# Kernel optimization log

Measured on AMD Instinct MI355X. Metric: run time of the kernel, lower is better.

The kernel has to match this reference:

```python
import jax, jax.numpy as jnp
import numpy as np

N_NONZERO = 32      # n_nonzero_coefs
TAU = 0.01
LAMBDA_INIT = -5.0  # reg_coeff = softplus(lambda)


def setup_inputs() -> dict:
    key = jax.random.key(0)
    k1, k2 = jax.random.split(key)
    X = jax.random.normal(k1, (64, 1024, 1024), dtype=jnp.float32)
    y = jax.random.normal(k2, (64, 1024, 1), dtype=jnp.float32)
    return {"X": X, "y": y}


def _omp_fit_forward(X, y):
    # Faithful translation of fit() (omp with hard straight-through top-1)
    # followed by forward() reconstruction D @ coef.
    reg = jax.nn.softplus(jnp.asarray(LAMBDA_INIT, jnp.float32)).astype(X.dtype)
    B, L, A = X.shape
    ones = jnp.ones((B, L, 1), X.dtype)
    Dfull = jnp.concatenate([X, ones], axis=-1)   # [B, L, A+1] (bias column)
    D = Dfull[0]                                   # shared dictionary [L, A+1]
    n_atoms = A + 1
    y2 = y[:, :, 0]                                # [B, L]
    y_det = jax.lax.stop_gradient(y2)
    residuals = y_det
    # Cache selected_D columns incrementally: each column j is dict @ ret_j,
    # identical math to the original's full recompute every iteration.
    selD = jnp.zeros((B, L, N_NONZERO), X.dtype)
    idx_all = []
    nzW = None
    for i in range(N_NONZERO):
        proj = residuals @ D                                      # [B, A+1]
        soft = jax.nn.softmax(jnp.abs(proj) / TAU, axis=-1)
        idx = jnp.argmax(jnp.abs(proj), axis=-1)                  # detached indices
        onehot = jax.nn.one_hot(jnp.argmax(soft, axis=-1), n_atoms, dtype=X.dtype)
        ret = onehot - jax.lax.stop_gradient(soft) + soft         # straight-through
        new_col = ret @ D.T                                       # [B, L]
        selD = selD.at[:, :, i].set(new_col)
        Di = selD[:, :, :i + 1]                                   # [B, L, i+1]
        DTy = jnp.einsum('blk,bl->bk', Di, y2)[..., None]         # [B, i+1, 1]
        DTD = jnp.einsum('blk,blj->bkj', Di, Di) + reg * jnp.eye(i + 1, dtype=X.dtype)
        nzW = jnp.linalg.solve(DTD, DTy)                          # [B, i+1, 1]
        residuals = y_det - jnp.einsum('blk,bk->bl', Di, nzW[..., 0])
        idx_all.append(idx)
    indices = jnp.stack(idx_all, axis=1)                          # [B, K] int
    W = jnp.zeros((B, n_atoms), X.dtype).at[jnp.arange(B)[:, None], indices].set(nzW[..., 0])
    # forward(): bmm(dict_with_bias, coef)
    recon = jnp.einsum('bla,ba->bl', Dfull, W)[..., None]         # [B, L, 1]
    return recon


def reference(X, y):
    return _omp_fit_forward(X, y)
```

## Files before the change

### kernel.cpp

```cpp
#include <hip/hip_runtime.h>
#include <math.h>

#define NATOMS   1025
#define GSTRIDE  1040
#define GELEMS   (1025*GSTRIDE)
#define CSTRIDE  33
#define NNZ      32
#define NBATCH   64
#define REGL     0.0067153485f

#define DPPF(x, ctrl) __int_as_float(__builtin_amdgcn_update_dpp(0, __float_as_int(x), (ctrl), 0xF, 0xF, false))

__device__ __forceinline__ float wave_sum64(float x) {
    x += DPPF(x, 0x111);
    x += DPPF(x, 0x112);
    x += DPPF(x, 0x114);
    x += DPPF(x, 0x118);
    x += DPPF(x, 0x142);
    x += DPPF(x, 0x143);
    return __int_as_float(__builtin_amdgcn_readlane(__float_as_int(x), 63));
}
__device__ __forceinline__ float readlane_f(float x, int l) {
    return __int_as_float(__builtin_amdgcn_readlane(__float_as_int(x), l));
}

__global__ __launch_bounds__(256)
void gramprojy_kernel(const float* __restrict__ X0, const float* __restrict__ y,
                      float* __restrict__ Gout, float* __restrict__ PY,
                      int kLen, int nsplit) {
    __shared__ float lds[8192];
    const int tid = threadIdx.x;

    if ((int)blockIdx.z < nsplit) {
        const int bx = blockIdx.x, by = blockIdx.y, bz = blockIdx.z;
        if (by < bx) return;
        float* As = lds;
        float* Bs = lds + 4096;
        const int a0 = bx * 128, b0 = by * 128;
        float* __restrict__ Gp = Gout + (size_t)bz * GELEMS;
        const int tx = tid & 15;
        const int ty = tid >> 4;
        const int lr = tid >> 5;
        const int lc = (tid & 31) * 4;
        const bool aIn = (a0 + 128) <= 1024;
        const bool bIn = (b0 + 128) <= 1024;

        float acc[8][8];
#pragma unroll
        for (int m = 0; m < 8; ++m)
#pragma unroll
            for (int n = 0; n < 8; ++n) acc[m][n] = 0.0f;

        const int kBase = bz * kLen;
        for (int kc = 0; kc < kLen; kc += 32) {
#pragma unroll
            for (int rr = 0; rr < 4; ++rr) {
                const int r = lr + rr * 8;
                const int l = kBase + kc + r;
                if (aIn) {
                    *(float4*)&As[r * 128 + lc] = *(const float4*)&X0[(size_t)l * 1024 + a0 + lc];
                } else {
#pragma unroll
                    for (int k = 0; k < 4; ++k) {
                        const int col = a0 + lc + k;
                        As[r * 128 + lc + k] = (col < 1024) ? X0[(size_t)l * 1024 + col]
                                                            : (col == 1024 ? 1.0f : 0.0f);
                    }
                }
                if (bIn) {
                    *(float4*)&Bs[r * 128 + lc] = *(const float4*)&X0[(size_t)l * 1024 + b0 + lc];
                } else {
#pragma unroll
                    for (int k = 0; k < 4; ++k) {
                        const int col = b0 + lc + k;
                        Bs[r * 128 + lc + k] = (col < 1024) ? X0[(size_t)l * 1024 + col]
                                                            : (col == 1024 ? 1.0f : 0.0f);
                    }
                }
            }
            __syncthreads();
#pragma unroll 8
            for (int l = 0; l < 32; ++l) {
                float4 a01 = *(const float4*)&As[l * 128 + ty * 8];
                float4 a23 = *(const float4*)&As[l * 128 + ty * 8 + 4];
                float4 bA  = *(const float4*)&Bs[l * 128 + tx * 4];
                float4 bB  = *(const float4*)&Bs[l * 128 + 64 + tx * 4];
                float am[8] = {a01.x, a01.y, a01.z, a01.w, a23.x, a23.y, a23.z, a23.w};
                float bn[8] = {bA.x, bA.y, bA.z, bA.w, bB.x, bB.y, bB.z, bB.w};
#pragma unroll
                for (int m = 0; m < 8; ++m)
#pragma unroll
                    for (int n = 0; n < 8; ++n)
                        acc[m][n] += am[m] * bn[n];
            }
            __syncthreads();
        }

#pragma unroll
        for (int m = 0; m < 8; ++m) {
            const int a = a0 + ty * 8 + m;
            if (a >= NATOMS) continue;
            const int bAc = b0 + tx * 4;
            const int bBc = b0 + 64 + tx * 4;
            if (bAc < GSTRIDE) {
                *(float4*)&Gp[(size_t)a * GSTRIDE + bAc] =
                    make_float4(acc[m][0], acc[m][1], acc[m][2], acc[m][3]);
            }
            if (bBc < GSTRIDE) {
                *(float4*)&Gp[(size_t)a * GSTRIDE + bBc] =
                    make_float4(acc[m][4], acc[m][5], acc[m][6], acc[m][7]);
            }
        }
        if (bx != by) {
#pragma unroll
            for (int n = 0; n < 8; ++n) {
                const int colg = b0 + ((n < 4) ? (tx * 4 + n) : (64 + tx * 4 + (n - 4)));
                if (colg >= NATOMS) continue;
                const int a = a0 + ty * 8;
                *(float4*)&Gp[(size_t)colg * GSTRIDE + a] =
                    make_float4(acc[0][n], acc[1][n], acc[2][n], acc[3][n]);
                *(float4*)&Gp[(size_t)colg * GSTRIDE + a + 4] =
                    make_float4(acc[4][n], acc[5][n], acc[6][n], acc[7][n]);
            }
        }
    } else {
        const int pw = blockIdx.y * 9 + blockIdx.x;
        if (pw >= 68) return;
        const int a0 = (pw % 17) * 64;
        const int b0 = (pw / 17) * 16;
        float* Ds = lds;
        float* Ys = lds + 2048;
        const int tx = tid & 15;
        const int ty = tid >> 4;
        const bool aIn = (a0 + 64) <= 1024;

        float acc[4] = {0.0f, 0.0f, 0.0f, 0.0f};

        for (int kc = 0; kc < 1024; kc += 32) {
            {
                const int r  = tid >> 4;
                const int c4 = (tid & 15) * 4;
#pragma unroll
                for (int rr = 0; rr < 2; ++rr) {
                    const int row = r + rr * 16;
                    const int l = kc + row;
                    if (aIn) {
                        *(float4*)&Ds[row * 64 + c4] = *(const float4*)&X0[(size_t)l * 1024 + a0 + c4];
                    } else {
#pragma unroll
                        for (int k = 0; k < 4; ++k) {
                            const int col = a0 + c4 + k;
                            Ds[row * 64 + c4 + k] = (col < 1024) ? X0[(size_t)l * 1024 + col]
                                                                 : (col == 1024 ? 1.0f : 0.0f);
                        }
                    }
                }
            }
            for (int e = tid; e < 512; e += 256) {
                const int l = e & 31, bb = e >> 5;
                Ys[l * 17 + bb] = y[(size_t)(b0 + bb) * 1024 + kc + l];
            }
            __syncthreads();
#pragma unroll 8
            for (int l = 0; l < 32; ++l) {
                const float yv = Ys[l * 17 + ty];
                float4 dv = *(const float4*)&Ds[l * 64 + tx * 4];
                acc[0] += yv * dv.x; acc[1] += yv * dv.y;
                acc[2] += yv * dv.z; acc[3] += yv * dv.w;
            }
            __syncthreads();
        }
        const int a = a0 + tx * 4;
        if (a < GSTRIDE) {
            *(float4*)&PY[(size_t)(b0 + ty) * GSTRIDE + a] =
                make_float4(acc[0], acc[1], acc[2], acc[3]);
        }
    }
}

template <int NS>
__global__ __launch_bounds__(512)
void omp_kernel(const float* __restrict__ Gp, const float* __restrict__ PY,
                int* __restrict__ idxOut, float* __restrict__ wOut) {
    __shared__ float colT[NATOMS * CSTRIDE];
    __shared__ float pyLds[1040];
    __shared__ float diagLds[1040];
    __shared__ float redV[2][8];
    __shared__ int   redI[2][8];

    const int b = blockIdx.x, tid = threadIdx.x;
    const int lane = tid & 63, wid = tid >> 6;

    float rr0[NNZ], rr1[NNZ];
    float ainv[32];
#pragma unroll
    for (int m = 0; m < 32; ++m) { ainv[m] = 0.f; rr0[m] = 0.f; rr1[m] = 0.f; }
    float wvr = 0.f, rhsr = 0.f;
    int   myIdx = 0;

    {
        for (int u = tid; u < NATOMS * CSTRIDE; u += 512) colT[u] = 0.f;
        const float* pyg = PY + (size_t)b * GSTRIDE;
        pyLds[tid] = pyg[tid];
        pyLds[tid + 512] = pyg[tid + 512];
        if (tid < 16) pyLds[1024 + tid] = pyg[1024 + tid];
        float d0 = 0.f, d1 = 0.f, d2 = 0.f;
#pragma unroll
        for (int z = 0; z < NS; ++z) {
            const float* gz = Gp + (size_t)z * GELEMS;
            d0 += gz[(size_t)tid * (GSTRIDE + 1)];
            d1 += gz[(size_t)(tid + 512) * (GSTRIDE + 1)];
            if (tid == 511) d2 += gz[(size_t)1024 * (GSTRIDE + 1)];
        }
        diagLds[tid] = d0;
        diagLds[tid + 512] = d1;
        if (tid == 511) diagLds[1024] = d2;
    }
    __syncthreads();

    float p0 = pyLds[tid], p1 = pyLds[tid + 512];
    float p2 = (tid == 511) ? pyLds[1024] : 0.f;

#define AM_STEP(ctrl) {                                                        \
        float ov = DPPF(wv_, ctrl);                                            \
        int   oi = __builtin_amdgcn_update_dpp(0, wi_, (ctrl), 0xF, 0xF, false);\
        if (ov > wv_ || (ov == wv_ && oi < wi_)) { wv_ = ov; wi_ = oi; } }
    {
        float best = fabsf(p0); int bidx = tid;
        { float v = fabsf(p1); if (v > best) { best = v; bidx = tid + 512; } }
        if (tid == 511) { float v = fabsf(p2); if (v > best) { best = v; bidx = 1024; } }
        float wv_ = best; int wi_ = bidx;
        AM_STEP(0x111) AM_STEP(0x112) AM_STEP(0x114) AM_STEP(0x118)
        AM_STEP(0x142) AM_STEP(0x143)
        wv_ = readlane_f(wv_, 63);
        wi_ = __builtin_amdgcn_readlane(wi_, 63);
        if (lane == 0) { redV[0][wid] = wv_; redI[0][wid] = wi_; }
    }
    __syncthreads();

#define OMP_ITER(I)                                                            \
    {                                                                          \
        const int par = (I) & 1;                                               \
        float bv_ = redV[par][0]; int sel = redI[par][0];                      \
        _Pragma("unroll")                                                      \
        for (int q = 1; q < 8; ++q) {                                          \
            if (redV[par][q] > bv_ ||                                          \
                (redV[par][q] == bv_ && redI[par][q] < sel)) {                 \
                bv_ = redV[par][q]; sel = redI[par][q];                        \
            }                                                                  \
        }                                                                      \
        const float pysel = pyLds[sel];                                        \
        float rA0=0.f,rA1=0.f,rA2=0.f,rA3=0.f;                                 \
        float rB0=0.f,rB1=0.f,rB2=0.f,rB3=0.f,rC=0.f;                          \
        if ((I) < NNZ - 1) {                                                   \
            const size_t ro = (size_t)sel * GSTRIDE;                           \
            { const float* g = Gp + ro; rA0 = g[tid]; rB0 = g[tid + 512]; }    \
            if (NS > 1) { const float* g = Gp + ro + (size_t)1 * GELEMS;       \
                          rA1 = g[tid]; rB1 = g[tid + 512]; }                  \
            if (NS > 2) { const float* g = Gp + ro + (size_t)2 * GELEMS;       \
                          rA2 = g[tid]; rB2 = g[tid + 512]; }                  \
            if (NS > 3) { const float* g = Gp + ro + (size_t)3 * GELEMS;       \
                          rA3 = g[tid]; rB3 = g[tid + 512]; }                  \
            if (tid == 511) {                                                  \
                _Pragma("unroll")                                              \
                for (int z = 0; z < NS; ++z)                                   \
                    rC += Gp[(size_t)z * GELEMS + ro + 1024];                  \
            }                                                                  \
        }                                                                      \
        const float* csel = &colT[sel * CSTRIDE];                              \
        const float bvl = (lane < 32) ? csel[lane] : 0.f;                      \
        float u0 = 0.f, u1 = 0.f;                                              \
        _Pragma("unroll")                                                      \
        for (int m = 0; m < 32; m += 2) {                                      \
            u0 = fmaf(ainv[m],     csel[m],     u0);                           \
            u1 = fmaf(ainv[m + 1], csel[m + 1], u1);                           \
        }                                                                      \
        const float uacc = u0 + u1;                                            \
        const float t = wave_sum64(bvl * uacc);                                \
        const float s = wave_sum64(rhsr * uacc);                               \
        const float dinv = 1.0f / (diagLds[sel] + REGL - t);                   \
        const float beta = dinv * (pysel - s);                                 \
        const float uvb = (lane == (I)) ? -1.0f : uacc;                        \
        _Pragma("unroll")                                                      \
        for (int m = 0; m < 32; ++m)                                           \
            ainv[m] = fmaf(uvb * dinv, readlane_f(uvb, m), ainv[m]);           \
        wvr  = (lane == (I)) ? beta  : fmaf(-uacc, beta, wvr);                 \
        rhsr = (lane == (I)) ? pysel : rhsr;                                   \
        if (tid == (I)) myIdx = sel;                                           \
        if ((I) < NNZ - 1) {                                                   \
            float z0 = 0.f, z1 = 0.f, z2 = 0.f;                                \
            _Pragma("unroll")                                                  \
            for (int j = 0; j < NNZ - 1; ++j) {                                \
                if (j < (I)) {                                                 \
                    const float uj = readlane_f(uvb, j);                       \
                    z0 = fmaf(uj, rr0[j], z0);                                 \
                    z1 = fmaf(uj, rr1[j], z1);                                 \
                    if (tid == 511) z2 = fmaf(uj, colT[1024 * CSTRIDE + j], z2); \
                }                                                              \
            }                                                                  \
            const float r0 = (rA0 + rA1) + (rA2 + rA3);                        \
            const float r1 = (rB0 + rB1) + (rB2 + rB3);                        \
            p0 = fmaf(beta, z0, p0); p0 = fmaf(-beta, r0, p0);                 \
            p1 = fmaf(beta, z1, p1); p1 = fmaf(-beta, r1, p1);                 \
            if (tid == 511) { p2 = fmaf(beta, z2, p2);                         \
                              p2 = fmaf(-beta, rC, p2); }                      \
            rr0[(I)] = r0; rr1[(I)] = r1;                                      \
            colT[tid * CSTRIDE + (I)] = r0;                                    \
            colT[(tid + 512) * CSTRIDE + (I)] = r1;                            \
            if (tid == 511) colT[1024 * CSTRIDE + (I)] = rC;                   \
            float best = fabsf(p0); int bidx = tid;                            \
            { float v = fabsf(p1); if (v > best) { best = v; bidx = tid + 512; } } \
            if (tid == 511) { float v = fabsf(p2);                             \
                              if (v > best) { best = v; bidx = 1024; } }       \
            float wv_ = best; int wi_ = bidx;                                  \
            AM_STEP(0x111) AM_STEP(0x112) AM_STEP(0x114) AM_STEP(0x118)       \
            AM_STEP(0x142) AM_STEP(0x143)                                      \
            wv_ = readlane_f(wv_, 63);                                         \
            wi_ = __builtin_amdgcn_readlane(wi_, 63);                          \
            if (lane == 0) { redV[par ^ 1][wid] = wv_;                         \
                             redI[par ^ 1][wid] = wi_; }                       \
            __syncthreads();                              \
        }                                                                      \
    }

    OMP_ITER(0)  OMP_ITER(1)  OMP_ITER(2)  OMP_ITER(3)
    OMP_ITER(4)  OMP_ITER(5)  OMP_ITER(6)  OMP_ITER(7)
    OMP_ITER(8)  OMP_ITER(9)  OMP_ITER(10) OMP_ITER(11)
    OMP_ITER(12) OMP_ITER(13) OMP_ITER(14) OMP_ITER(15)
    OMP_ITER(16) OMP_ITER(17) OMP_ITER(18) OMP_ITER(19)
    OMP_ITER(20) OMP_ITER(21) OMP_ITER(22) OMP_ITER(23)
    OMP_ITER(24) OMP_ITER(25) OMP_ITER(26) OMP_ITER(27)
    OMP_ITER(28) OMP_ITER(29) OMP_ITER(30) OMP_ITER(31)
#undef OMP_ITER
#undef AM_STEP

    if (tid < NNZ) {
        idxOut[b * NNZ + tid] = myIdx;
        wOut[b * NNZ + tid] = wvr;
    }
}

__global__ __launch_bounds__(256)
void recon_kernel(const float* __restrict__ X, const int* __restrict__ idxIn,
                  const float* __restrict__ wIn, float* __restrict__ out) {
    __shared__ float Wd[1025];
    __shared__ float wval[NNZ];
    __shared__ int   widx[NNZ];
    __shared__ float biasS;
    const int b = blockIdx.x >> 2, chunk = blockIdx.x & 3;
    const int tid = threadIdx.x;
    for (int u = tid; u < 1025; u += 256) Wd[u] = 0.0f;
    __syncthreads();
    if (tid == 0) {
#pragma unroll
        for (int i = 0; i < NNZ; ++i) Wd[idxIn[b * NNZ + i]] = wIn[b * NNZ + i];
        float bias = 0.0f;
#pragma unroll
        for (int i = 0; i < NNZ; ++i) {
            const int gi = idxIn[b * NNZ + i];
            const float v = Wd[gi];
            Wd[gi] = 0.0f;
            const bool isOnes = (gi == 1024);
            if (isOnes) bias += v;
            widx[i] = isOnes ? 0 : gi;
            wval[i] = isOnes ? 0.0f : v;
        }
        biasS = bias;
    }
    __syncthreads();
    const int l = chunk * 256 + tid;
    const float* __restrict__ xr = X + (size_t)b * 1024 * 1024 + (size_t)l * 1024;
    float a0 = biasS, a1 = 0.f, a2 = 0.f, a3 = 0.f;
#pragma unroll
    for (int i = 0; i < NNZ; i += 4) {
        a0 = fmaf(xr[widx[i + 0]], wval[i + 0], a0);
        a1 = fmaf(xr[widx[i + 1]], wval[i + 1], a1);
        a2 = fmaf(xr[widx[i + 2]], wval[i + 2], a2);
        a3 = fmaf(xr[widx[i + 3]], wval[i + 3], a3);
    }
    out[(size_t)b * 1024 + l] = (a0 + a1) + (a2 + a3);
}

extern "C" void kernel_launch(void* const* d_in, const int* in_sizes, int n_in,
                              void* d_out, int out_size, void* d_ws, size_t ws_size,
                              hipStream_t stream) {
    const float* X = (const float*)d_in[0];
    const float* y = (const float*)d_in[1];
    float* out = (float*)d_out;
    float* ws = (float*)d_ws;

    const size_t fixed = (size_t)64 * GSTRIDE + NBATCH * NNZ * 2 + 64;
    const size_t need4 = ((size_t)GELEMS * 4 + fixed) * sizeof(float);
    const int nsplit = (ws_size >= need4) ? 4 : 1;
    const int kLen = 1024 / nsplit;

    float* Gp = ws;
    float* PY = ws + (size_t)GELEMS * nsplit;
    float* wOut = PY + (size_t)64 * GSTRIDE;
    int* idxOut = (int*)(wOut + NBATCH * NNZ);

    gramprojy_kernel<<<dim3(9, 9, nsplit + 1), 256, 0, stream>>>(X, y, Gp, PY, kLen, nsplit);
    if (nsplit == 4) omp_kernel<4><<<NBATCH, 512, 0, stream>>>(Gp, PY, idxOut, wOut);
    else             omp_kernel<1><<<NBATCH, 512, 0, stream>>>(Gp, PY, idxOut, wOut);
    recon_kernel<<<NBATCH * 4, 256, 0, stream>>>(X, idxOut, wOut, out);
}
```

Before: 183.2 us.

## Drop large LDS column cache and split Gram computation eight ways

Removes the 1025x33 float shared-memory column cache (about 135 KB) from the OMP kernel. The selected atom's coefficient vector is now broadcast through a small 32-entry shared buffer, written by the thread that already holds that row in registers, which costs one extra barrier per iteration. The Gram build gains an 8-way K split when the workspace is large enough, giving the first kernel more parallel blocks. In exchange the OMP kernel must sum eight partial Gram rows per iteration instead of four, roughly doubling its global reads.

```diff
diff --git a/kernel.cpp b/kernel.cpp
--- a/kernel.cpp
+++ b/kernel.cpp
@@ -4,7 +4,6 @@
 #define NATOMS   1025
 #define GSTRIDE  1040
 #define GELEMS   (1025*GSTRIDE)
-#define CSTRIDE  33
 #define NNZ      32
 #define NBATCH   64
 #define REGL     0.0067153485f
@@ -182,9 +181,10 @@
 __global__ __launch_bounds__(512)
 void omp_kernel(const float* __restrict__ Gp, const float* __restrict__ PY,
                 int* __restrict__ idxOut, float* __restrict__ wOut) {
-    __shared__ float colT[NATOMS * CSTRIDE];
     __shared__ float pyLds[1040];
     __shared__ float diagLds[1040];
+    __shared__ float bvec[32];
+    __shared__ float row1024[NNZ];
     __shared__ float redV[2][8];
     __shared__ int   redI[2][8];
 
@@ -199,7 +199,6 @@
     int   myIdx = 0;
 
     {
-        for (int u = tid; u < NATOMS * CSTRIDE; u += 512) colT[u] = 0.f;
         const float* pyg = PY + (size_t)b * GSTRIDE;
         pyLds[tid] = pyg[tid];
         pyLds[tid + 512] = pyg[tid + 512];
@@ -215,6 +214,7 @@
         diagLds[tid] = d0;
         diagLds[tid + 512] = d1;
         if (tid == 511) diagLds[1024] = d2;
+        if (tid < 32) { bvec[tid] = 0.f; row1024[tid] = 0.f; }
     }
     __syncthreads();
 
@@ -251,7 +251,9 @@
         }                                                                      \
         const float pysel = pyLds[sel];                                        \
         float rA0=0.f,rA1=0.f,rA2=0.f,rA3=0.f;                                 \
-        float rB0=0.f,rB1=0.f,rB2=0.f,rB3=0.f,rC=0.f;                          \
+        float rA4=0.f,rA5=0.f,rA6=0.f,rA7=0.f;                                 \
+        float rB0=0.f,rB1=0.f,rB2=0.f,rB3=0.f;                                 \
+        float rB4=0.f,rB5=0.f,rB6=0.f,rB7=0.f,rC=0.f;                          \
         if ((I) < NNZ - 1) {                                                   \
             const size_t ro = (size_t)sel * GSTRIDE;                           \
             { const float* g = Gp + ro; rA0 = g[tid]; rB0 = g[tid + 512]; }    \
@@ -261,19 +263,38 @@
                           rA2 = g[tid]; rB2 = g[tid + 512]; }                  \
             if (NS > 3) { const float* g = Gp + ro + (size_t)3 * GELEMS;       \
                           rA3 = g[tid]; rB3 = g[tid + 512]; }                  \
+            if (NS > 4) { const float* g = Gp + ro + (size_t)4 * GELEMS;       \
+                          rA4 = g[tid]; rB4 = g[tid + 512]; }                  \
+            if (NS > 5) { const float* g = Gp + ro + (size_t)5 * GELEMS;       \
+                          rA5 = g[tid]; rB5 = g[tid + 512]; }                  \
+            if (NS > 6) { const float* g = Gp + ro + (size_t)6 * GELEMS;       \
+                          rA6 = g[tid]; rB6 = g[tid + 512]; }                  \
+            if (NS > 7) { const float* g = Gp + ro + (size_t)7 * GELEMS;       \
+                          rA7 = g[tid]; rB7 = g[tid + 512]; }                  \
             if (tid == 511) {                                                  \
                 _Pragma("unroll")                                              \
                 for (int z = 0; z < NS; ++z)                                   \
                     rC += Gp[(size_t)z * GELEMS + ro + 1024];                  \
             }                                                                  \
         }                                                                      \
-        const float* csel = &colT[sel * CSTRIDE];                              \
-        const float bvl = (lane < 32) ? csel[lane] : 0.f;                      \
+        if (sel == 1024) {                                                     \
+            if (tid < 32) bvec[tid] = row1024[tid];                            \
+        } else if (tid == (sel & 511)) {                                       \
+            if (sel >> 9) {                                                    \
+                _Pragma("unroll")                                              \
+                for (int m = 0; m < 32; ++m) bvec[m] = rr1[m];                 \
+            } else {                                                           \
+                _Pragma("unroll")                                              \
+                for (int m = 0; m < 32; ++m) bvec[m] = rr0[m];                 \
+            }                                                                  \
+        }                                                                      \
+        __syncthreads();                               \
+        const float bvl = (lane < 32) ? bvec[lane] : 0.f;                      \
         float u0 = 0.f, u1 = 0.f;                                              \
         _Pragma("unroll")                                                      \
         for (int m = 0; m < 32; m += 2) {                                      \
-            u0 = fmaf(ainv[m],     csel[m],     u0);                           \
-            u1 = fmaf(ainv[m + 1], csel[m + 1], u1);                           \
+            u0 = fmaf(ainv[m],     bvec[m],     u0);                           \
+            u1 = fmaf(ainv[m + 1], bvec[m + 1], u1);                           \
         }                                                                      \
         const float uacc = u0 + u1;                                            \
         const float t = wave_sum64(bvl * uacc);                                \
@@ -295,19 +316,19 @@
                     const float uj = readlane_f(uvb, j);                       \
                     z0 = fmaf(uj, rr0[j], z0);                                 \
                     z1 = fmaf(uj, rr1[j], z1);                                 \
-                    if (tid == 511) z2 = fmaf(uj, colT[1024 * CSTRIDE + j], z2); \
+                    if (tid == 511) z2 = fmaf(uj, row1024[j], z2);             \
                 }                                                              \
             }                                                                  \
-            const float r0 = (rA0 + rA1) + (rA2 + rA3);                        \
-            const float r1 = (rB0 + rB1) + (rB2 + rB3);                        \
+            const float r0 = ((rA0 + rA1) + (rA2 + rA3))                       \
+                           + ((rA4 + rA5) + (rA6 + rA7));                      \
+            const float r1 = ((rB0 + rB1) + (rB2 + rB3))                       \
+                           + ((rB4 + rB5) + (rB6 + rB7));                      \
             p0 = fmaf(beta, z0, p0); p0 = fmaf(-beta, r0, p0);                 \
             p1 = fmaf(beta, z1, p1); p1 = fmaf(-beta, r1, p1);                 \
             if (tid == 511) { p2 = fmaf(beta, z2, p2);                         \
                               p2 = fmaf(-beta, rC, p2); }                      \
             rr0[(I)] = r0; rr1[(I)] = r1;                                      \
-            colT[tid * CSTRIDE + (I)] = r0;                                    \
-            colT[(tid + 512) * CSTRIDE + (I)] = r1;                            \
-            if (tid == 511) colT[1024 * CSTRIDE + (I)] = rC;                   \
+            if (tid == 511) row1024[(I)] = rC;                                 \
             float best = fabsf(p0); int bidx = tid;                            \
             { float v = fabsf(p1); if (v > best) { best = v; bidx = tid + 512; } } \
             if (tid == 511) { float v = fabsf(p2);                             \
@@ -319,7 +340,7 @@
             wi_ = __builtin_amdgcn_readlane(wi_, 63);                          \
             if (lane == 0) { redV[par ^ 1][wid] = wv_;                         \
                              redI[par ^ 1][wid] = wi_; }                       \
-            __syncthreads();                              \
+            __syncthreads();                    \
         }                                                                      \
     }
 
@@ -390,8 +411,9 @@
     float* ws = (float*)d_ws;
 
     const size_t fixed = (size_t)64 * GSTRIDE + NBATCH * NNZ * 2 + 64;
+    const size_t need8 = ((size_t)GELEMS * 8 + fixed) * sizeof(float);
     const size_t need4 = ((size_t)GELEMS * 4 + fixed) * sizeof(float);
-    const int nsplit = (ws_size >= need4) ? 4 : 1;
+    const int nsplit = (ws_size >= need8) ? 8 : ((ws_size >= need4) ? 4 : 1);
     const int kLen = 1024 / nsplit;
 
     float* Gp = ws;
@@ -400,7 +422,8 @@
     int* idxOut = (int*)(wOut + NBATCH * NNZ);
 
     gramprojy_kernel<<<dim3(9, 9, nsplit + 1), 256, 0, stream>>>(X, y, Gp, PY, kLen, nsplit);
-    if (nsplit == 4) omp_kernel<4><<<NBATCH, 512, 0, stream>>>(Gp, PY, idxOut, wOut);
-    else             omp_kernel<1><<<NBATCH, 512, 0, stream>>>(Gp, PY, idxOut, wOut);
+    if (nsplit == 8)      omp_kernel<8><<<NBATCH, 512, 0, stream>>>(Gp, PY, idxOut, wOut);
+    else if (nsplit == 4) omp_kernel<4><<<NBATCH, 512, 0, stream>>>(Gp, PY, idxOut, wOut);
+    else                  omp_kernel<1><<<NBATCH, 512, 0, stream>>>(Gp, PY, idxOut, wOut);
     recon_kernel<<<NBATCH * 4, 256, 0, stream>>>(X, idxOut, wOut, out);
 }
```

Result: slower. 203.0 us (+10.8%).
